# Kernel tuning notes

Measured on AMD Instinct MI355X. Metric: run time of the kernel, lower is better.

The kernel has to match this reference:

```python
import jax, jax.numpy as jnp
import numpy as np

DIM = 1024
N_HEADS = 16
HEAD_DIM = DIM // N_HEADS  # 64
B, T = 4, 2048


def setup_inputs() -> dict:
    key = jax.random.key(0)
    ks = jax.random.split(key, 6)
    x = jax.random.normal(ks[0], (B, T, DIM), dtype=jnp.float32)
    # causal mask; original does att.masked_fill(mask == 0, -inf)
    mask = jnp.tril(jnp.ones((T, T), dtype=bool))[None, None, :, :]
    s = 1.0 / np.sqrt(DIM)
    Wq = jax.random.normal(ks[1], (DIM, DIM), dtype=jnp.float32) * s
    Wk = jax.random.normal(ks[2], (DIM, DIM), dtype=jnp.float32) * s
    Wv = jax.random.normal(ks[3], (DIM, DIM), dtype=jnp.float32) * s
    Wo = jax.random.normal(ks[4], (DIM, DIM), dtype=jnp.float32) * s
    bo = jnp.zeros((DIM,), dtype=jnp.float32)
    return {"x": x, "mask": mask, "Wq": Wq, "Wk": Wk, "Wv": Wv,
            "Wo": Wo, "bo": bo, "start_pos": 0}


def reference(x, mask, Wq, Wk, Wv, Wo, bo, start_pos):
    Bx, Tx, C = x.shape
    # torch nn.Linear: y = x @ W.T (no bias for QKV)
    q = jnp.einsum('btc,dc->btd', x, Wq).reshape(Bx, Tx, N_HEADS, HEAD_DIM)
    k = jnp.einsum('btc,dc->btd', x, Wk).reshape(Bx, Tx, N_HEADS, HEAD_DIM)
    v = jnp.einsum('btc,dc->btd', x, Wv).reshape(Bx, Tx, N_HEADS, HEAD_DIM)
    # no caching path: keys=k, values=v
    scale = 1.0 / jnp.sqrt(jnp.asarray(HEAD_DIM, dtype=x.dtype))
    # [B, H, Tq, Tk]
    att = jnp.einsum('bqhd,bkhd->bhqk', q, k) * scale
    att = jnp.where(mask, att, jnp.asarray(-jnp.inf, dtype=att.dtype))
    att = jax.nn.softmax(att, axis=-1)
    out = jnp.einsum('bhqk,bkhd->bqhd', att, v).reshape(Bx, Tx, C)
    return jnp.einsum('btc,dc->btd', out, Wo) + bo
```

## Files before the change

### kernel.cpp

```cpp
#include <hip/hip_runtime.h>
#include <cstdint>
#include <cstddef>

typedef __bf16 bf16;
typedef bf16 bf16x8 __attribute__((ext_vector_type(8)));
typedef float f32x4 __attribute__((ext_vector_type(4)));
typedef float f32x16 __attribute__((ext_vector_type(16)));

__device__ inline f32x4 mfma_16x16x32(bf16x8 a, bf16x8 b, f32x4 c) {
    return __builtin_amdgcn_mfma_f32_16x16x32_bf16(a, b, c, 0, 0, 0);
}
__device__ inline f32x16 mfma_32x32x16(bf16x8 a, bf16x8 b, f32x16 c) {
    return __builtin_amdgcn_mfma_f32_32x32x16_bf16(a, b, c, 0, 0, 0);
}
__device__ inline uint32_t cvt_pk_bf16(float lo, float hi) {
    uint32_t r;
    asm("v_cvt_pk_bf16_f32 %0, %1, %2" : "=v"(r) : "v"(lo), "v"(hi));
    return r;
}

#define GLD16(gsrc, ldst)                                                              \
    __builtin_amdgcn_global_load_lds(                                                  \
        (const __attribute__((address_space(1))) uint32_t*)(gsrc),                     \
        (__attribute__((address_space(3))) uint32_t*)(ldst), 16, 0, 0)

__global__ void cvt_all(const float* __restrict__ x,
                        const float* __restrict__ w0, const float* __restrict__ w1,
                        const float* __restrict__ w2, const float* __restrict__ w3,
                        bf16* __restrict__ xb,
                        bf16* __restrict__ d0, bf16* __restrict__ d1,
                        bf16* __restrict__ d2, bf16* __restrict__ d3) {
    const int id = blockIdx.x;
    const float* src;
    bf16* dst;
    int boff;
    if (id < 8192) {
        src = x; dst = xb; boff = id;
    } else {
        const int r = id - 8192;
        const int z = r >> 10;
        boff = r & 1023;
        src = (z == 0) ? w0 : (z == 1) ? w1 : (z == 2) ? w2 : w3;
        dst = (z == 0) ? d0 : (z == 1) ? d1 : (z == 2) ? d2 : d3;
    }
    const size_t i = ((size_t)boff * 256 + threadIdx.x) * 4;
    float4 f = *(const float4*)(src + i);
    union { bf16 o4[4]; uint2 u; } pk;
    pk.o4[0] = (bf16)f.x; pk.o4[1] = (bf16)f.y; pk.o4[2] = (bf16)f.z; pk.o4[3] = (bf16)f.w;
    *(uint2*)(dst + i) = pk.u;
}

#define BM 128
#define BN 128
#define BK 64
#define QSCALE 0.18033688011112042f

__global__ __launch_bounds__(256, 2)
void gemm_qkv(const bf16* __restrict__ xb,
              const bf16* __restrict__ wq, const bf16* __restrict__ wk, const bf16* __restrict__ wv,
              bf16* __restrict__ qo, bf16* __restrict__ ko, bf16* __restrict__ vo)
{
    __shared__ bf16 sA[BM][BK];
    __shared__ bf16 sB[BN][BK];
    const int K = 1024;
    const int tid = threadIdx.x;
    const int lane = tid & 63, wave = tid >> 6;
    const int wm = wave >> 1, wn = wave & 1;
    const int quad = lane >> 4, ln = lane & 15;
    const int lr = lane >> 3;
    const int ssc = ((lane & 7) ^ lr) * 8;
    const int lnm = ln & 7;
    const int rc0 = (quad ^ lnm) * 8;
    const int rc1 = ((4 | quad) ^ lnm) * 8;
    const int id = blockIdx.x;
    const int z = id >> 9;
    const int xt = (id & 511) >> 6;
    const int yt = id & 63;
    const bf16* W = (z == 0) ? wq : (z == 1) ? wk : wv;
    const int row0 = yt * BM;
    const int col0 = xt * BN;

    f32x4 acc[4][4];
    const f32x4 zero = {0.f, 0.f, 0.f, 0.f};
#pragma unroll
    for (int i = 0; i < 4; ++i)
#pragma unroll
        for (int j = 0; j < 4; ++j) acc[i][j] = zero;

    for (int k0 = 0; k0 < K; k0 += BK) {
#pragma unroll
        for (int s = 0; s < 4; ++s) {
            int ra = wave * 32 + s * 8;
            GLD16(&xb[(size_t)(row0 + ra + lr) * K + k0 + ssc], &sA[ra][0]);
            GLD16(&W [(size_t)(col0 + ra + lr) * K + k0 + ssc], &sB[ra][0]);
        }
        __syncthreads();
#pragma unroll
        for (int kk = 0; kk < BK; kk += 32) {
            const int rc = kk ? rc1 : rc0;
            bf16x8 af[4], bfv[4];
#pragma unroll
            for (int i = 0; i < 4; ++i) {
                af[i]  = *(const bf16x8*)(&sA[wm * 64 + i * 16 + ln][rc]);
                bfv[i] = *(const bf16x8*)(&sB[wn * 64 + i * 16 + ln][rc]);
            }
#pragma unroll
            for (int mi = 0; mi < 4; ++mi)
#pragma unroll
                for (int ni = 0; ni < 4; ++ni)
                    acc[mi][ni] = mfma_16x16x32(af[mi], bfv[ni], acc[mi][ni]);
        }
        __syncthreads();
    }
    if (z == 2) {
#pragma unroll
        for (int mi = 0; mi < 4; ++mi)
#pragma unroll
            for (int ni = 0; ni < 4; ++ni) {
                int gm0 = row0 + wm * 64 + mi * 16 + quad * 4;
                int gn = col0 + wn * 64 + ni * 16 + ln;
                int b = gm0 >> 11, t = gm0 & 2047;
                int h = gn >> 6,  d = gn & 63;
                union { bf16 v[4]; uint2 u; } pk;
#pragma unroll
                for (int i = 0; i < 4; ++i) pk.v[i] = (bf16)acc[mi][ni][i];
                *(uint2*)(&vo[((size_t)((b * 16 + h) * 64 + d)) * 2048 + t]) = pk.u;
            }
    } else {
        const float scale = (z == 0) ? QSCALE : 1.0f;
        bf16* outp = (z == 0) ? qo : ko;
#pragma unroll
        for (int mi = 0; mi < 4; ++mi)
#pragma unroll
            for (int ni = 0; ni < 4; ++ni)
#pragma unroll
                for (int i = 0; i < 4; ++i) {
                    int gm = row0 + wm * 64 + mi * 16 + quad * 4 + i;
                    int gn = col0 + wn * 64 + ni * 16 + ln;
                    int b = gm >> 11, t = gm & 2047;
                    int h = gn >> 6,  d = gn & 63;
                    outp[((size_t)((b * 16 + h) * 2048 + t)) * 64 + d] = (bf16)(acc[mi][ni][i] * scale);
                }
    }
}

__global__ __launch_bounds__(256, 2)
void gemm_out(const bf16* __restrict__ ab, const bf16* __restrict__ wo,
              const float* __restrict__ bias, float* __restrict__ out)
{
    __shared__ bf16 sA[BM][BK];
    __shared__ bf16 sB[BN][BK];
    const int K = 1024;
    const int tid = threadIdx.x;
    const int lane = tid & 63, wave = tid >> 6;
    const int wm = wave >> 1, wn = wave & 1;
    const int quad = lane >> 4, ln = lane & 15;
    const int lr = lane >> 3;
    const int ssc = ((lane & 7) ^ lr) * 8;
    const int lnm = ln & 7;
    const int rc0 = (quad ^ lnm) * 8;
    const int rc1 = ((4 | quad) ^ lnm) * 8;
    const int id = blockIdx.x;
    const int xt = id >> 6, yt = id & 63;
    const int row0 = yt * BM;
    const int col0 = xt * BN;

    f32x4 acc[4][4];
    const f32x4 zero = {0.f, 0.f, 0.f, 0.f};
#pragma unroll
    for (int i = 0; i < 4; ++i)
#pragma unroll
        for (int j = 0; j < 4; ++j) acc[i][j] = zero;

    for (int k0 = 0; k0 < K; k0 += BK) {
#pragma unroll
        for (int s = 0; s < 4; ++s) {
            int ra = wave * 32 + s * 8;
            GLD16(&ab[(size_t)(row0 + ra + lr) * K + k0 + ssc], &sA[ra][0]);
            GLD16(&wo[(size_t)(col0 + ra + lr) * K + k0 + ssc], &sB[ra][0]);
        }
        __syncthreads();
#pragma unroll
        for (int kk = 0; kk < BK; kk += 32) {
            const int rc = kk ? rc1 : rc0;
            bf16x8 af[4], bfv[4];
#pragma unroll
            for (int i = 0; i < 4; ++i) {
                af[i]  = *(const bf16x8*)(&sA[wm * 64 + i * 16 + ln][rc]);
                bfv[i] = *(const bf16x8*)(&sB[wn * 64 + i * 16 + ln][rc]);
            }
#pragma unroll
            for (int mi = 0; mi < 4; ++mi)
#pragma unroll
                for (int ni = 0; ni < 4; ++ni)
                    acc[mi][ni] = mfma_16x16x32(af[mi], bfv[ni], acc[mi][ni]);
        }
        __syncthreads();
    }
#pragma unroll
    for (int mi = 0; mi < 4; ++mi)
#pragma unroll
        for (int ni = 0; ni < 4; ++ni)
#pragma unroll
            for (int i = 0; i < 4; ++i) {
                int gm = row0 + wm * 64 + mi * 16 + quad * 4 + i;
                int gn = col0 + wn * 64 + ni * 16 + ln;
                out[(size_t)gm * 1024 + gn] = acc[mi][ni][i] + bias[gn];
            }
}

__global__ __launch_bounds__(256, 2)
void flash_attn(const bf16* __restrict__ q, const bf16* __restrict__ k,
                const bf16* __restrict__ vt, bf16* __restrict__ ao)
{
    __shared__ bf16 sK[64][72];
    __shared__ bf16 sV[64][72];
    const int tid = threadIdx.x, lane = tid & 63, w = tid >> 6;
    const int c31 = lane & 31, hi = lane >> 5, hi8 = hi * 8;
    const int id = blockIdx.x;
    const int bh = id & 63;
    const int q0 = (15 - (id >> 6)) * 128;
    const size_t base = (size_t)bh * (2048 * 64);
    const int sr = tid >> 3, sc = (tid & 7) * 8;
    const int rw = q0 + w * 32;
    const int rw31 = rw + 31;
    const int qrow = rw + c31;

    bf16x8 qf[4];
#pragma unroll
    for (int dt = 0; dt < 4; ++dt)
        qf[dt] = *(const bf16x8*)(&q[base + (size_t)qrow * 64 + dt * 16 + hi8]);

    const f32x16 z16 = {0.f,0.f,0.f,0.f,0.f,0.f,0.f,0.f,0.f,0.f,0.f,0.f,0.f,0.f,0.f,0.f};
    f32x16 o0 = z16, o1 = z16;
    float lsum = 0.f;

    const int kend = q0 + 128;
    uint4 rKa = *(const uint4*)(&k [base + (size_t)sr * 64 + sc]);
    uint4 rKb = *(const uint4*)(&k [base + (size_t)(sr + 32) * 64 + sc]);
    uint4 rVa = *(const uint4*)(&vt[base + (size_t)sr * 2048 + sc]);
    uint4 rVb = *(const uint4*)(&vt[base + (size_t)(sr + 32) * 2048 + sc]);

    for (int k0 = 0; k0 < kend; k0 += 64) {
        __syncthreads();
        *(uint4*)(&sK[sr][sc])      = rKa;
        *(uint4*)(&sK[sr + 32][sc]) = rKb;
        *(uint4*)(&sV[sr][sc])      = rVa;
        *(uint4*)(&sV[sr + 32][sc]) = rVb;
        __syncthreads();
        if (k0 + 64 < kend) {
            int kn = k0 + 64;
            rKa = *(const uint4*)(&k [base + (size_t)(kn + sr) * 64 + sc]);
            rKb = *(const uint4*)(&k [base + (size_t)(kn + sr + 32) * 64 + sc]);
            rVa = *(const uint4*)(&vt[base + (size_t)sr * 2048 + kn + sc]);
            rVb = *(const uint4*)(&vt[base + (size_t)(sr + 32) * 2048 + kn + sc]);
        }
        if (k0 <= rw31) {
#pragma unroll
            for (int kt = 0; kt < 2; ++kt) {
                const int ktb = k0 + kt * 32;
                if (ktb <= rw31) {
                    bf16x8 kf0 = *(const bf16x8*)(&sK[kt * 32 + c31][ 0 + hi8]);
                    bf16x8 kf1 = *(const bf16x8*)(&sK[kt * 32 + c31][16 + hi8]);
                    bf16x8 kf2 = *(const bf16x8*)(&sK[kt * 32 + c31][32 + hi8]);
                    bf16x8 kf3 = *(const bf16x8*)(&sK[kt * 32 + c31][48 + hi8]);
                    f32x16 st = z16;
                    st = mfma_32x32x16(kf0, qf[0], st);
                    st = mfma_32x32x16(kf1, qf[1], st);
                    st = mfma_32x32x16(kf2, qf[2], st);
                    st = mfma_32x32x16(kf3, qf[3], st);
                    const int kb2 = ktb + hi * 4;
                    if (ktb + 31 > rw) {
#pragma unroll
                        for (int r = 0; r < 16; ++r) {
                            int kk = kb2 + (r & 3) + 8 * (r >> 2);
                            if (kk > qrow) st[r] = -INFINITY;
                        }
                    }
                    float pp[16];
                    float ps = 0.f;
#pragma unroll
                    for (int r = 0; r < 16; ++r) {
                        float p = __builtin_amdgcn_exp2f(st[r]);
                        ps += p;
                        pp[r] = p;
                    }
                    lsum += ps;
#pragma unroll
                    for (int ks = 0; ks < 2; ++ks) {
                        const int ob = ks * 8;
                        uint32_t a0 = cvt_pk_bf16(pp[ob + 0], pp[ob + 1]);
                        uint32_t a1 = cvt_pk_bf16(pp[ob + 2], pp[ob + 3]);
                        uint32_t a2 = cvt_pk_bf16(pp[ob + 4], pp[ob + 5]);
                        uint32_t a3 = cvt_pk_bf16(pp[ob + 6], pp[ob + 7]);
                        auto r02 = __builtin_amdgcn_permlane32_swap(a0, a2, false, false);
                        auto r13 = __builtin_amdgcn_permlane32_swap(a1, a3, false, false);
                        union { uint32_t u[4]; bf16x8 v; } af;
                        af.u[0] = r02[0]; af.u[1] = r13[0];
                        af.u[2] = r02[1]; af.u[3] = r13[1];
                        const int co = kt * 32 + ks * 16 + hi8;
                        bf16x8 v0 = *(const bf16x8*)(&sV[c31][co]);
                        bf16x8 v1 = *(const bf16x8*)(&sV[32 + c31][co]);
                        o0 = mfma_32x32x16(v0, af.v, o0);
                        o1 = mfma_32x32x16(v1, af.v, o1);
                    }
                }
            }
        }
    }

    float l = lsum + __shfl_xor(lsum, 32);
    const float inv = 1.0f / l;
    const int b = bh >> 4, h = bh & 15;
    bf16* orow = &ao[(size_t)(b * 2048 + qrow) * 1024 + h * 64];
#pragma unroll
    for (int g = 0; g < 4; ++g) {
        union { bf16 v4[4]; uint2 u; } pk0, pk1;
#pragma unroll
        for (int i = 0; i < 4; ++i) {
            pk0.v4[i] = (bf16)(o0[g * 4 + i] * inv);
            pk1.v4[i] = (bf16)(o1[g * 4 + i] * inv);
        }
        *(uint2*)(&orow[     g * 8 + hi * 4]) = pk0.u;
        *(uint2*)(&orow[32 + g * 8 + hi * 4]) = pk1.u;
    }
}

extern "C" void kernel_launch(void* const* d_in, const int* in_sizes, int n_in,
                              void* d_out, int out_size, void* d_ws, size_t ws_size,
                              hipStream_t stream) {
    const float* x  = (const float*)d_in[0];
    const float* Wq = (const float*)d_in[2];
    const float* Wk = (const float*)d_in[3];
    const float* Wv = (const float*)d_in[4];
    const float* Wo = (const float*)d_in[5];
    const float* bo = (const float*)d_in[6];
    float* out = (float*)d_out;

    char* p = (char*)d_ws;
    const size_t MK = 8192ull * 1024;
    bf16* xb  = (bf16*)p; p += MK * 2;
    bf16* wqb = (bf16*)p; p += (1ull << 20) * 2;
    bf16* wkb = (bf16*)p; p += (1ull << 20) * 2;
    bf16* wvb = (bf16*)p; p += (1ull << 20) * 2;
    bf16* wob = (bf16*)p; p += (1ull << 20) * 2;
    bf16* qb  = (bf16*)p; p += MK * 2;
    bf16* kb  = (bf16*)p; p += MK * 2;
    bf16* vtb = (bf16*)p; p += MK * 2;
    bf16* aob = (bf16*)p; p += MK * 2;

    cvt_all<<<12288, 256, 0, stream>>>(x, Wq, Wk, Wv, Wo, xb, wqb, wkb, wvb, wob);

    gemm_qkv<<<1536, 256, 0, stream>>>(xb, wqb, wkb, wvb, qb, kb, vtb);
    flash_attn<<<1024, 256, 0, stream>>>(qb, kb, vtb, aob);
    gemm_out<<<512, 256, 0, stream>>>(aob, wob, bo, out);
}
```

Baseline: 228.5 us.

## Rewrite QKV GEMM with 256x256 tiles, double-buffered LDS, and interleaved MFMA phases

```diff
diff --git a/kernel.cpp b/kernel.cpp
--- a/kernel.cpp
+++ b/kernel.cpp
@@ -50,22 +50,19 @@
     *(uint2*)(dst + i) = pk.u;
 }
 
-#define BM 128
-#define BN 128
-#define BK 64
 #define QSCALE 0.18033688011112042f
 
-__global__ __launch_bounds__(256, 2)
+__global__ __launch_bounds__(512, 2)
 void gemm_qkv(const bf16* __restrict__ xb,
               const bf16* __restrict__ wq, const bf16* __restrict__ wk, const bf16* __restrict__ wv,
               bf16* __restrict__ qo, bf16* __restrict__ ko, bf16* __restrict__ vo)
 {
-    __shared__ bf16 sA[BM][BK];
-    __shared__ bf16 sB[BN][BK];
-    const int K = 1024;
+    extern __shared__ char smem[];
+    bf16 (*sA)[256][64] = (bf16 (*)[256][64])smem;
+    bf16 (*sB)[256][64] = (bf16 (*)[256][64])(smem + 2 * 256 * 64 * 2);
     const int tid = threadIdx.x;
     const int lane = tid & 63, wave = tid >> 6;
-    const int wm = wave >> 1, wn = wave & 1;
+    const int wm = wave >> 2, wn = wave & 3;
     const int quad = lane >> 4, ln = lane & 15;
     const int lr = lane >> 3;
     const int ssc = ((lane & 7) ^ lr) * 8;
@@ -73,77 +70,165 @@
     const int rc0 = (quad ^ lnm) * 8;
     const int rc1 = ((4 | quad) ^ lnm) * 8;
     const int id = blockIdx.x;
-    const int z = id >> 9;
-    const int xt = (id & 511) >> 6;
-    const int yt = id & 63;
+    const int z = id >> 7;
+    const int xt = (id & 127) >> 5;
+    const int yt = id & 31;
     const bf16* W = (z == 0) ? wq : (z == 1) ? wk : wv;
-    const int row0 = yt * BM;
-    const int col0 = xt * BN;
-
-    f32x4 acc[4][4];
+    const int row0 = yt * 256;
+    const int col0 = xt * 256;
+    const int srow = tid >> 3;
+    const int ldsr = wave * 8;
+    const bf16* aS = xb + (size_t)(row0 + srow) * 1024 + ssc;
+    const bf16* bS = W  + (size_t)(col0 + srow) * 1024 + ssc;
+
+    f32x4 acc[8][4];
     const f32x4 zero = {0.f, 0.f, 0.f, 0.f};
 #pragma unroll
-    for (int i = 0; i < 4; ++i)
+    for (int i = 0; i < 8; ++i)
 #pragma unroll
         for (int j = 0; j < 4; ++j) acc[i][j] = zero;
 
-    for (int k0 = 0; k0 < K; k0 += BK) {
-#pragma unroll
-        for (int s = 0; s < 4; ++s) {
-            int ra = wave * 32 + s * 8;
-            GLD16(&xb[(size_t)(row0 + ra + lr) * K + k0 + ssc], &sA[ra][0]);
-            GLD16(&W [(size_t)(col0 + ra + lr) * K + k0 + ssc], &sB[ra][0]);
-        }
-        __syncthreads();
-#pragma unroll
-        for (int kk = 0; kk < BK; kk += 32) {
-            const int rc = kk ? rc1 : rc0;
-            bf16x8 af[4], bfv[4];
-#pragma unroll
-            for (int i = 0; i < 4; ++i) {
-                af[i]  = *(const bf16x8*)(&sA[wm * 64 + i * 16 + ln][rc]);
-                bfv[i] = *(const bf16x8*)(&sB[wn * 64 + i * 16 + ln][rc]);
-            }
-#pragma unroll
-            for (int mi = 0; mi < 4; ++mi)
-#pragma unroll
-                for (int ni = 0; ni < 4; ++ni)
-                    acc[mi][ni] = mfma_16x16x32(af[mi], bfv[ni], acc[mi][ni]);
-        }
-        __syncthreads();
-    }
+#define STA(tn) do { const int cb_ = (tn) & 1; const size_t ko_ = (size_t)(tn) * 64;  \
+    GLD16(aS +            ko_, &sA[cb_][      ldsr][0]);                              \
+    GLD16(aS +  64*1024 + ko_, &sA[cb_][ 64 + ldsr][0]);                              \
+    GLD16(aS + 128*1024 + ko_, &sA[cb_][128 + ldsr][0]);                              \
+    GLD16(aS + 192*1024 + ko_, &sA[cb_][192 + ldsr][0]); } while (0)
+#define STB(tn) do { const int cb_ = (tn) & 1; const size_t ko_ = (size_t)(tn) * 64;  \
+    GLD16(bS +            ko_, &sB[cb_][      ldsr][0]);                              \
+    GLD16(bS +  64*1024 + ko_, &sB[cb_][ 64 + ldsr][0]);                              \
+    GLD16(bS + 128*1024 + ko_, &sB[cb_][128 + ldsr][0]);                              \
+    GLD16(bS + 192*1024 + ko_, &sB[cb_][192 + ldsr][0]); } while (0)
+
+#define LGKM0_FENCE                                                           \
+    asm volatile("s_waitcnt lgkmcnt(0)" ::: "memory");                        \
+    __builtin_amdgcn_sched_barrier(0);
+
+#define QITER(T, DOSTAGE, EVM) do {                                           \
+    const int cur_ = (T) & 1;                                                 \
+    bf16x8 a0_[4][2], a1_[4][2], b0_[2][2], b1_[2][2];                        \
+                                        \
+    _Pragma("unroll")                                                         \
+    for (int mi = 0; mi < 4; ++mi) {                                          \
+        a0_[mi][0] = *(const bf16x8*)(&sA[cur_][wm * 128 + mi * 16 + ln][rc0]); \
+        a0_[mi][1] = *(const bf16x8*)(&sA[cur_][wm * 128 + mi * 16 + ln][rc1]); \
+    }                                                                         \
+    _Pragma("unroll")                                                         \
+    for (int ni = 0; ni < 2; ++ni) {                                          \
+        b0_[ni][0] = *(const bf16x8*)(&sB[cur_][wn * 64 + ni * 16 + ln][rc0]); \
+        b0_[ni][1] = *(const bf16x8*)(&sB[cur_][wn * 64 + ni * 16 + ln][rc1]); \
+    }                                                                         \
+    __builtin_amdgcn_s_barrier();                                             \
+    LGKM0_FENCE                                                               \
+    __builtin_amdgcn_s_setprio(1);                                            \
+    _Pragma("unroll")                                                         \
+    for (int mi = 0; mi < 4; ++mi)                                            \
+        _Pragma("unroll")                                                     \
+        for (int ni = 0; ni < 2; ++ni) {                                      \
+            acc[mi][ni] = mfma_16x16x32(a0_[mi][0], b0_[ni][0], acc[mi][ni]); \
+            acc[mi][ni] = mfma_16x16x32(a0_[mi][1], b0_[ni][1], acc[mi][ni]); \
+        }                                                                     \
+    __builtin_amdgcn_s_setprio(0);                                            \
+    __builtin_amdgcn_s_barrier();                                             \
+                                         \
+    _Pragma("unroll")                                                         \
+    for (int mi = 0; mi < 4; ++mi) {                                          \
+        a1_[mi][0] = *(const bf16x8*)(&sA[cur_][wm * 128 + 64 + mi * 16 + ln][rc0]); \
+        a1_[mi][1] = *(const bf16x8*)(&sA[cur_][wm * 128 + 64 + mi * 16 + ln][rc1]); \
+    }                                                                         \
+    __builtin_amdgcn_s_barrier();                                             \
+    LGKM0_FENCE                                                               \
+    __builtin_amdgcn_s_setprio(1);                                            \
+    _Pragma("unroll")                                                         \
+    for (int mi = 0; mi < 4; ++mi)                                            \
+        _Pragma("unroll")                                                     \
+        for (int ni = 0; ni < 2; ++ni) {                                      \
+            acc[4 + mi][ni] = mfma_16x16x32(a1_[mi][0], b0_[ni][0], acc[4 + mi][ni]); \
+            acc[4 + mi][ni] = mfma_16x16x32(a1_[mi][1], b0_[ni][1], acc[4 + mi][ni]); \
+        }                                                                     \
+    __builtin_amdgcn_s_setprio(0);                                            \
+    __builtin_amdgcn_s_barrier();                                             \
+     \
+    _Pragma("unroll")                                                         \
+    for (int ni = 0; ni < 2; ++ni) {                                          \
+        b1_[ni][0] = *(const bf16x8*)(&sB[cur_][wn * 64 + 32 + ni * 16 + ln][rc0]); \
+        b1_[ni][1] = *(const bf16x8*)(&sB[cur_][wn * 64 + 32 + ni * 16 + ln][rc1]); \
+    }                                                                         \
+    if (DOSTAGE) { STA((T) + 2); }                                            \
+    __builtin_amdgcn_s_barrier();                                             \
+    LGKM0_FENCE                                                               \
+    __builtin_amdgcn_s_setprio(1);                                            \
+    _Pragma("unroll")                                                         \
+    for (int mi = 0; mi < 4; ++mi)                                            \
+        _Pragma("unroll")                                                     \
+        for (int ni = 0; ni < 2; ++ni) {                                      \
+            acc[4 + mi][2 + ni] = mfma_16x16x32(a1_[mi][0], b1_[ni][0], acc[4 + mi][2 + ni]); \
+            acc[4 + mi][2 + ni] = mfma_16x16x32(a1_[mi][1], b1_[ni][1], acc[4 + mi][2 + ni]); \
+        }                                                                     \
+    __builtin_amdgcn_s_setprio(0);                                            \
+    __builtin_amdgcn_s_barrier();                                             \
+     \
+    if (DOSTAGE) { STB((T) + 2); }                                            \
+    __builtin_amdgcn_s_barrier();                                             \
+    __builtin_amdgcn_s_setprio(1);                                            \
+    _Pragma("unroll")                                                         \
+    for (int mi = 0; mi < 4; ++mi)                                            \
+        _Pragma("unroll")                                                     \
+        for (int ni = 0; ni < 2; ++ni) {                                      \
+            acc[mi][2 + ni] = mfma_16x16x32(a0_[mi][0], b1_[ni][0], acc[mi][2 + ni]); \
+            acc[mi][2 + ni] = mfma_16x16x32(a0_[mi][1], b1_[ni][1], acc[mi][2 + ni]); \
+        }                                                                     \
+    __builtin_amdgcn_s_setprio(0);                                            \
+    if ((EVM) == 8)      asm volatile("s_waitcnt vmcnt(8)" ::: "memory");     \
+    else if ((EVM) == 0) asm volatile("s_waitcnt vmcnt(0)" ::: "memory");     \
+    __builtin_amdgcn_s_barrier();                                             \
+} while (0)
+
+    STA(0); STB(0); STA(1); STB(1);
+    asm volatile("s_waitcnt vmcnt(8)" ::: "memory");
+    __builtin_amdgcn_s_barrier();
+#pragma unroll 2
+    for (int t = 0; t < 14; ++t) { QITER(t, 1, 8); }
+    QITER(14, 0, 0);
+    QITER(15, 0, -1);
+
     if (z == 2) {
 #pragma unroll
-        for (int mi = 0; mi < 4; ++mi)
-#pragma unroll
-            for (int ni = 0; ni < 4; ++ni) {
-                int gm0 = row0 + wm * 64 + mi * 16 + quad * 4;
-                int gn = col0 + wn * 64 + ni * 16 + ln;
+        for (int i = 0; i < 8; ++i)
+#pragma unroll
+            for (int j = 0; j < 4; ++j) {
+                int gm0 = row0 + wm * 128 + (i >> 2) * 64 + (i & 3) * 16 + quad * 4;
+                int gn = col0 + wn * 64 + (j >> 1) * 32 + (j & 1) * 16 + ln;
                 int b = gm0 >> 11, t = gm0 & 2047;
                 int h = gn >> 6,  d = gn & 63;
                 union { bf16 v[4]; uint2 u; } pk;
 #pragma unroll
-                for (int i = 0; i < 4; ++i) pk.v[i] = (bf16)acc[mi][ni][i];
+                for (int e = 0; e < 4; ++e) pk.v[e] = (bf16)acc[i][j][e];
                 *(uint2*)(&vo[((size_t)((b * 16 + h) * 64 + d)) * 2048 + t]) = pk.u;
             }
     } else {
         const float scale = (z == 0) ? QSCALE : 1.0f;
         bf16* outp = (z == 0) ? qo : ko;
 #pragma unroll
-        for (int mi = 0; mi < 4; ++mi)
-#pragma unroll
-            for (int ni = 0; ni < 4; ++ni)
-#pragma unroll
-                for (int i = 0; i < 4; ++i) {
-                    int gm = row0 + wm * 64 + mi * 16 + quad * 4 + i;
-                    int gn = col0 + wn * 64 + ni * 16 + ln;
+        for (int i = 0; i < 8; ++i)
+#pragma unroll
+            for (int j = 0; j < 4; ++j)
+#pragma unroll
+                for (int e = 0; e < 4; ++e) {
+                    int gm = row0 + wm * 128 + (i >> 2) * 64 + (i & 3) * 16 + quad * 4 + e;
+                    int gn = col0 + wn * 64 + (j >> 1) * 32 + (j & 1) * 16 + ln;
                     int b = gm >> 11, t = gm & 2047;
                     int h = gn >> 6,  d = gn & 63;
-                    outp[((size_t)((b * 16 + h) * 2048 + t)) * 64 + d] = (bf16)(acc[mi][ni][i] * scale);
+                    outp[((size_t)((b * 16 + h) * 2048 + t)) * 64 + d] = (bf16)(acc[i][j][e] * scale);
                 }
     }
-}
-
+#undef STA
+#undef STB
+#undef QITER
+}
+
+#define BM 128
+#define BN 128
+#define BK 64
 __global__ __launch_bounds__(256, 2)
 void gemm_out(const bf16* __restrict__ ab, const bf16* __restrict__ wo,
               const float* __restrict__ bias, float* __restrict__ out)
@@ -349,9 +434,16 @@
     bf16* vtb = (bf16*)p; p += MK * 2;
     bf16* aob = (bf16*)p; p += MK * 2;
 
+    static bool attr_done = false;
+    if (!attr_done) {
+        hipFuncSetAttribute(reinterpret_cast<const void*>(&gemm_qkv),
+                            hipFuncAttributeMaxDynamicSharedMemorySize, 131072);
+        attr_done = true;
+    }
+
     cvt_all<<<12288, 256, 0, stream>>>(x, Wq, Wk, Wv, Wo, xb, wqb, wkb, wvb, wob);
 
-    gemm_qkv<<<1536, 256, 0, stream>>>(xb, wqb, wkb, wvb, qb, kb, vtb);
+    gemm_qkv<<<384, 512, 131072, stream>>>(xb, wqb, wkb, wvb, qb, kb, vtb);
     flash_attn<<<1024, 256, 0, stream>>>(qb, kb, vtb, aob);
     gemm_out<<<512, 256, 0, stream>>>(aob, wob, bo, out);
 }
```

Measured after the change: 246.7 us. 1.08x slower.
